# Kernel optimization log

Hardware: AMD Instinct MI355X
Metric: run time of the kernel (lower is better)

The kernel has to match this reference:

```python
import jax, jax.numpy as jnp
import numpy as np


def setup_inputs() -> dict:
    key = jax.random.key(0)
    ks = jax.random.split(key, 8)
    B, C, H, W = 8, 256, 64, 64
    Cqk = C // 8
    x = jax.random.normal(ks[0], (B, C, H, W), dtype=jnp.float32)
    # 1x1 conv weights, stored as [out_ch, in_ch] (kernel is 1x1)
    Wq = jax.random.normal(ks[1], (Cqk, C), dtype=jnp.float32) * 0.02
    bq = jnp.zeros((Cqk,), dtype=jnp.float32)
    Wk = jax.random.normal(ks[2], (Cqk, C), dtype=jnp.float32) * 0.02
    bk = jnp.zeros((Cqk,), dtype=jnp.float32)
    Wv = jax.random.normal(ks[3], (C, C), dtype=jnp.float32) * 0.02
    bv = jnp.zeros((C,), dtype=jnp.float32)
    # gamma initialized to zero in the module; use small nonzero so grads flow through attention path meaningfully
    gamma = jnp.asarray([0.5], dtype=jnp.float32)
    return {"x": x, "Wq": Wq, "bq": bq, "Wk": Wk, "bk": bk, "Wv": Wv, "bv": bv, "gamma": gamma}


def reference(x, Wq, bq, Wk, bk, Wv, bv, gamma):
    B, C, H, W = x.shape
    N = H * W
    xf = x.reshape(B, C, N)  # [B, C, N]
    # 1x1 convs == channel-wise matmuls
    q = jnp.einsum('oc,bcn->bno', Wq, xf) + bq  # [B, N, Cqk]
    k = jnp.einsum('oc,bcn->bon', Wk, xf) + bk[None, :, None]  # [B, Cqk, N]
    v = jnp.einsum('oc,bcn->bon', Wv, xf) + bv[None, :, None]  # [B, C, N]
    energy = jnp.einsum('bnd,bdm->bnm', q, k)  # [B, N, N], unscaled as in original
    attn = jax.nn.softmax(energy, axis=-1)
    out = jnp.einsum('bcm,bnm->bcn', v, attn)  # out[:, :, n] = sum_m v[:, :, m] * attn[n, m]
    out = out.reshape(B, C, H, W)
    return gamma[0] * out + x
```

## Files before the change

### kernel.cpp

```cpp
#include <hip/hip_runtime.h>
#include <hip/hip_bf16.h>

#define NB 8
#define CH 256
#define NN 4096
#define CQK 32
#define LOG2E 1.4426950408889634f

typedef __attribute__((ext_vector_type(4))) float f32x4;
typedef __attribute__((ext_vector_type(16))) float f32x16;
typedef __attribute__((ext_vector_type(8))) short bf16x8;
typedef unsigned short u16;

static __device__ __forceinline__ u16 f2bf(float f) {
  unsigned int u = __float_as_uint(f);
  unsigned int r = (u + 0x7fffu + ((u >> 16) & 1u)) >> 16;
  return (u16)r;
}

__global__ void prep_weights(const float* __restrict__ Wq, const float* __restrict__ bq,
                             const float* __restrict__ Wk, const float* __restrict__ bk,
                             const float* __restrict__ Wv,
                             u16* __restrict__ Wqkf, u16* __restrict__ Wvf,
                             float* __restrict__ bqk) {
  int i = blockIdx.x * 256 + threadIdx.x;
  int o = i >> 8, c = i & 255;
  int kk = c >> 5, g2 = (c >> 3) & 3, j = c & 7;
  if (o < 64) {
    float wv = (o < 32) ? Wq[o * 256 + c] * LOG2E : Wk[(o - 32) * 256 + c];
    Wqkf[((((o >> 4) * 8 + kk) * 4 + g2) * 16 + (o & 15)) * 8 + j] = f2bf(wv);
  }
  Wvf[((((o >> 4) * 8 + kk) * 4 + g2) * 16 + (o & 15)) * 8 + j] = f2bf(Wv[i]);
  if (i < 64) bqk[i] = (i < 32) ? bq[i] * LOG2E : bk[i - 32];
}

__global__ __launch_bounds__(256, 2) void fused_proj(
    const float* __restrict__ x, const u16* __restrict__ Wqkf,
    const u16* __restrict__ Wvf, const float* __restrict__ bqk,
    const float* __restrict__ bv,
    u16* __restrict__ qbuf, u16* __restrict__ kbuf, u16* __restrict__ vbuf) {
  __shared__ __align__(128) char xt[64 * 512];
  const int b = blockIdx.y, n0 = blockIdx.x * 64;
  const int tid = threadIdx.x, w = tid >> 6, l = tid & 63, g = l >> 4, lr = l & 15;
  const f32x4 fzero = {0.f, 0.f, 0.f, 0.f};

  {
    const int nl = l, cl = w;
    const float* xp = x + (size_t)b * CH * NN + n0 + nl;
    char* xrow = xt + nl * 512;
    const int swz = (nl & 15) << 4;
#pragma unroll
    for (int p = 0; p < 32; ++p) {
      const int c = p * 8 + cl * 2;
      float f0 = xp[(size_t)c * NN], f1 = xp[(size_t)(c + 1) * NN];
      unsigned int pk = (unsigned int)f2bf(f0) | ((unsigned int)f2bf(f1) << 16);
      *(unsigned int*)(xrow + ((c * 2) ^ swz)) = pk;
    }
  }
  __syncthreads();

  const int aswz = lr << 4;

  {
    f32x4 acc[4];
#pragma unroll
    for (int ct = 0; ct < 4; ++ct) acc[ct] = fzero;
#pragma unroll
    for (int kk = 0; kk < 8; ++kk) {
      bf16x8 af = *(const bf16x8*)(xt + (w * 16 + lr) * 512 + ((kk * 64 + g * 16) ^ aswz));
#pragma unroll
      for (int ct = 0; ct < 4; ++ct) {
        bf16x8 bf = *(const bf16x8*)(Wqkf + (size_t)(((ct * 8 + kk) * 4 + g) * 16 + lr) * 8);
        acc[ct] = __builtin_amdgcn_mfma_f32_16x16x32_bf16(af, bf, acc[ct], 0, 0, 0);
      }
    }
#pragma unroll
    for (int ct = 0; ct < 4; ++ct) {
      const int col = ct * 16 + lr;
      const float bc = bqk[col];
#pragma unroll
      for (int r = 0; r < 4; ++r) {
        const int row = n0 + w * 16 + g * 4 + r;
        u16 h = f2bf(acc[ct][r] + bc);
        if (col < 32) qbuf[((size_t)(b * NN + row)) * 32 + col] = h;
        else          kbuf[((size_t)(b * NN + row)) * 32 + (col - 32)] = h;
      }
    }
  }

  {
    f32x4 vacc[4][4];
#pragma unroll
    for (int ct = 0; ct < 4; ++ct)
#pragma unroll
      for (int mt = 0; mt < 4; ++mt) vacc[ct][mt] = fzero;
#pragma unroll
    for (int kk = 0; kk < 8; ++kk) {
      bf16x8 bfm[4];
#pragma unroll
      for (int mt = 0; mt < 4; ++mt)
        bfm[mt] = *(const bf16x8*)(xt + (mt * 16 + lr) * 512 + ((kk * 64 + g * 16) ^ aswz));
#pragma unroll
      for (int ct = 0; ct < 4; ++ct) {
        bf16x8 af = *(const bf16x8*)(Wvf + (size_t)((((w * 4 + ct) * 8 + kk) * 4 + g) * 16 + lr) * 8);
#pragma unroll
        for (int mt = 0; mt < 4; ++mt)
          vacc[ct][mt] = __builtin_amdgcn_mfma_f32_16x16x32_bf16(af, bfm[mt], vacc[ct][mt], 0, 0, 0);
      }
    }
#pragma unroll
    for (int ct = 0; ct < 4; ++ct) {
#pragma unroll
      for (int mt = 0; mt < 4; ++mt) {
        const int m = n0 + mt * 16 + lr;
#pragma unroll
        for (int r = 0; r < 4; ++r) {
          const int ch = w * 64 + ct * 16 + g * 4 + r;
          vbuf[((size_t)(b * 128 + (m >> 5)) * 256 + ch) * 32 + (m & 31)] = f2bf(vacc[ct][mt][r] + bv[ch]);
        }
      }
    }
  }
}

#define KLOAD(t, sub) (*(const bf16x8*)(kp + (size_t)((((t) & 63) * 64) + (sub) * 16) * 32))
#define VLOAD32(mg, k16) (*(const bf16x8*)(vp32 + (size_t)((mg) & 127) * 8192 + (k16)))

#define EXPP(S, PW, MASK) {                                                                   \
  float e0 = __builtin_amdgcn_exp2f(S[0]);                                                    \
  float e1 = __builtin_amdgcn_exp2f(S[1]);                                                    \
  float e2 = __builtin_amdgcn_exp2f(S[2]);                                                    \
  float e3 = __builtin_amdgcn_exp2f(S[3]);                                                    \
  lsum += (MASK) * ((e0 + e1) + (e2 + e3));                                                   \
  PW.x = __builtin_amdgcn_perm(__float_as_uint(e1) + 0x8000u, __float_as_uint(e0) + 0x8000u, 0x07060302u); \
  PW.y = __builtin_amdgcn_perm(__float_as_uint(e3) + 0x8000u, __float_as_uint(e2) + 0x8000u, 0x07060302u); \
}

#define PBAR() do {                                  \
  __builtin_amdgcn_sched_barrier(0);                 \
  asm volatile("s_waitcnt lgkmcnt(0)");              \
  __builtin_amdgcn_s_barrier();                      \
  __builtin_amdgcn_sched_barrier(0);                 \
} while (0)

#define PVPHASE32(BUF, V00, V01, V10, V11) {                                                  \
  const char* prb = (const char*)Pb + (BUF) * 16384;                                          \
  char* pdst = (char*)Pb + ((BUF) ^ 1) * 16384 + prow * 128;                                  \
  *(uint2*)(pdst + ((0 * 32 + g * 8) ^ wswz)) = pw0;                                          \
  *(uint2*)(pdst + ((1 * 32 + g * 8) ^ wswz)) = pw1;                                          \
  *(uint2*)(pdst + ((2 * 32 + g * 8) ^ wswz)) = pw2;                                          \
  *(uint2*)(pdst + ((3 * 32 + g * 8) ^ wswz)) = pw3;                                          \
  __builtin_amdgcn_s_setprio(1);                                                              \
  _Pragma("unroll")                                                                           \
  for (int qt = 0; qt < 4; ++qt) {                                                            \
    const int row = qt * 32 + (l & 31);                                                       \
    const int rs = (row & 7) << 4;                                                            \
    const char* base = prb + row * 128;                                                       \
    bf16x8 p00 = *(const bf16x8*)(base + ((0 + hi16) ^ rs));                                  \
    bf16x8 p01 = *(const bf16x8*)(base + ((32 + hi16) ^ rs));                                 \
    bf16x8 p10 = *(const bf16x8*)(base + ((64 + hi16) ^ rs));                                 \
    bf16x8 p11 = *(const bf16x8*)(base + ((96 + hi16) ^ rs));                                 \
    oacc32[qt] = __builtin_amdgcn_mfma_f32_32x32x16_bf16(V00, p00, oacc32[qt], 0, 0, 0);      \
    oacc32[qt] = __builtin_amdgcn_mfma_f32_32x32x16_bf16(V01, p01, oacc32[qt], 0, 0, 0);      \
    oacc32[qt] = __builtin_amdgcn_mfma_f32_32x32x16_bf16(V10, p10, oacc32[qt], 0, 0, 0);      \
    oacc32[qt] = __builtin_amdgcn_mfma_f32_32x32x16_bf16(V11, p11, oacc32[qt], 0, 0, 0);      \
  }                                                                                           \
  __builtin_amdgcn_s_setprio(0);                                                              \
}

__global__ __launch_bounds__(512, 2) void attn_fused(
    const u16* __restrict__ qb, const u16* __restrict__ kbuf,
    const u16* __restrict__ vbuf, const float* __restrict__ x,
    const float* __restrict__ gamma_p, float* __restrict__ out) {
  __shared__ __align__(128) char Pb[2][128 * 128];
  __shared__ float lsum_s[128];

  const int b = blockIdx.x;
  const int n0 = blockIdx.y * 128;
  const int tid = threadIdx.x, w = tid >> 6, l = tid & 63, g = l >> 4, lr = l & 15;
  const float gamma0 = gamma_p[0];
  const f32x4 fzero = {0.f, 0.f, 0.f, 0.f};
  const int hi16 = (l >> 5) << 4;

  bf16x8 qf = *(const bf16x8*)(qb + ((size_t)b * NN + n0 + w * 16 + lr) * 32 + g * 8);

  const u16* kp = kbuf + (size_t)b * (NN * 32) + (size_t)lr * 32 + g * 8;
  const u16* vp32 = vbuf + (size_t)b * 1048576 + (size_t)(w * 32 + (l & 31)) * 32 + (l >> 5) * 8;

  f32x16 oacc32[4];
#pragma unroll
  for (int qt = 0; qt < 4; ++qt) oacc32[qt] = (f32x16){};
  float lsum = 0.f;

  const int prow = w * 16 + lr;
  const int wswz = (prow & 7) << 4;

  bf16x8 kA0 = KLOAD(0, 0), kA1 = KLOAD(0, 1), kA2 = KLOAD(0, 2), kA3 = KLOAD(0, 3);
  bf16x8 vA0 = VLOAD32(0, 0), vA1 = VLOAD32(0, 16), vA2 = VLOAD32(1, 0), vA3 = VLOAD32(1, 16);
  bf16x8 kB0 = KLOAD(1, 0), kB1 = KLOAD(1, 1), kB2 = KLOAD(1, 2), kB3 = KLOAD(1, 3);
  bf16x8 vB0, vB1, vB2, vB3;
  uint2 pw0, pw1, pw2, pw3;
  {
    f32x4 s0 = __builtin_amdgcn_mfma_f32_16x16x32_bf16(kA0, qf, fzero, 0, 0, 0);
    f32x4 s1 = __builtin_amdgcn_mfma_f32_16x16x32_bf16(kA1, qf, fzero, 0, 0, 0);
    f32x4 s2 = __builtin_amdgcn_mfma_f32_16x16x32_bf16(kA2, qf, fzero, 0, 0, 0);
    f32x4 s3 = __builtin_amdgcn_mfma_f32_16x16x32_bf16(kA3, qf, fzero, 0, 0, 0);
    EXPP(s0, pw0, 1.0f); EXPP(s1, pw1, 1.0f); EXPP(s2, pw2, 1.0f); EXPP(s3, pw3, 1.0f);
    char* pdst = (char*)Pb + prow * 128;
    *(uint2*)(pdst + ((0 * 32 + g * 8) ^ wswz)) = pw0;
    *(uint2*)(pdst + ((1 * 32 + g * 8) ^ wswz)) = pw1;
    *(uint2*)(pdst + ((2 * 32 + g * 8) ^ wswz)) = pw2;
    *(uint2*)(pdst + ((3 * 32 + g * 8) ^ wswz)) = pw3;
  }

  for (int it2 = 0; it2 < 32; ++it2) {
    {
      const int tn = 2 * it2 + 1;
      f32x4 s0 = __builtin_amdgcn_mfma_f32_16x16x32_bf16(kB0, qf, fzero, 0, 0, 0);
      f32x4 s1 = __builtin_amdgcn_mfma_f32_16x16x32_bf16(kB1, qf, fzero, 0, 0, 0);
      f32x4 s2 = __builtin_amdgcn_mfma_f32_16x16x32_bf16(kB2, qf, fzero, 0, 0, 0);
      f32x4 s3 = __builtin_amdgcn_mfma_f32_16x16x32_bf16(kB3, qf, fzero, 0, 0, 0);
      kA0 = KLOAD(tn + 1, 0); kA1 = KLOAD(tn + 1, 1); kA2 = KLOAD(tn + 1, 2); kA3 = KLOAD(tn + 1, 3);
      vB0 = VLOAD32(2 * tn, 0); vB1 = VLOAD32(2 * tn, 16);
      vB2 = VLOAD32(2 * tn + 1, 0); vB3 = VLOAD32(2 * tn + 1, 16);
      EXPP(s0, pw0, 1.0f); EXPP(s1, pw1, 1.0f); EXPP(s2, pw2, 1.0f); EXPP(s3, pw3, 1.0f);
      PBAR();
      PVPHASE32(0, vA0, vA1, vA2, vA3);
    }
    {
      const int tn = 2 * it2 + 2;
      const float tmask = (it2 < 31) ? 1.0f : 0.0f;
      f32x4 s0 = __builtin_amdgcn_mfma_f32_16x16x32_bf16(kA0, qf, fzero, 0, 0, 0);
      f32x4 s1 = __builtin_amdgcn_mfma_f32_16x16x32_bf16(kA1, qf, fzero, 0, 0, 0);
      f32x4 s2 = __builtin_amdgcn_mfma_f32_16x16x32_bf16(kA2, qf, fzero, 0, 0, 0);
      f32x4 s3 = __builtin_amdgcn_mfma_f32_16x16x32_bf16(kA3, qf, fzero, 0, 0, 0);
      kB0 = KLOAD(tn + 1, 0); kB1 = KLOAD(tn + 1, 1); kB2 = KLOAD(tn + 1, 2); kB3 = KLOAD(tn + 1, 3);
      vA0 = VLOAD32(2 * tn, 0); vA1 = VLOAD32(2 * tn, 16);
      vA2 = VLOAD32(2 * tn + 1, 0); vA3 = VLOAD32(2 * tn + 1, 16);
      EXPP(s0, pw0, tmask); EXPP(s1, pw1, tmask); EXPP(s2, pw2, tmask); EXPP(s3, pw3, tmask);
      PBAR();
      PVPHASE32(1, vB0, vB1, vB2, vB3);
    }
  }

  lsum += __shfl_xor(lsum, 16);
  lsum += __shfl_xor(lsum, 32);
  if (l < 16) lsum_s[w * 16 + lr] = lsum;
  __syncthreads();

  const size_t bbase = (size_t)b * CH * NN;
#pragma unroll
  for (int qt = 0; qt < 4; ++qt) {
    const int q = qt * 32 + (l & 31);
    const float linv = 1.f / lsum_s[q];
    const int n = n0 + q;
#pragma unroll
    for (int a = 0; a < 4; ++a) {
#pragma unroll
      for (int rr = 0; rr < 4; ++rr) {
        const int ch = w * 32 + rr + a * 8 + 4 * (l >> 5);
        const size_t off = bbase + (size_t)ch * NN + n;
        out[off] = gamma0 * (oacc32[qt][a * 4 + rr] * linv) + x[off];
      }
    }
  }
}

extern "C" void kernel_launch(void* const* d_in, const int* in_sizes, int n_in,
                              void* d_out, int out_size, void* d_ws, size_t ws_size,
                              hipStream_t stream) {
  const float* x     = (const float*)d_in[0];
  const float* Wq    = (const float*)d_in[1];
  const float* bq    = (const float*)d_in[2];
  const float* Wk    = (const float*)d_in[3];
  const float* bk    = (const float*)d_in[4];
  const float* Wv    = (const float*)d_in[5];
  const float* bv    = (const float*)d_in[6];
  const float* gamma = (const float*)d_in[7];
  float* out = (float*)d_out;

  char* ws = (char*)d_ws;
  u16*   qbuf = (u16*)(ws);
  u16*   kbuf = (u16*)(ws + 2097152);
  u16*   vbuf = (u16*)(ws + 4194304);
  u16*   Wqkf = (u16*)(ws + 20971520);
  u16*   Wvf  = (u16*)(ws + 21004288);
  float* bqk  = (float*)(ws + 21135360);

  prep_weights<<<256, 256, 0, stream>>>(Wq, bq, Wk, bk, Wv, Wqkf, Wvf, bqk);
  fused_proj<<<dim3(64, 8), 256, 0, stream>>>(x, Wqkf, Wvf, bqk, bv, qbuf, kbuf, vbuf);
  attn_fused<<<dim3(8, 32), 512, 0, stream>>>(qbuf, kbuf, vbuf, x, gamma, out);
}
```

Before: 115.1 us.

## Retile PV stage to 16x16x32 MFMA with 2x4 wave grid over queries and channels

The PV product moves from 32x32x16 MFMAs, where each wave owned 32 channels across all 128 query rows, to 16x16x32 MFMAs over a 2x4 wave grid: 64 query rows by 64 channels per wave. Each P fragment read from LDS is now reused across four channel tiles, and V is loaded per channel tile, with the next V group's loads issued mid-phase. The goal is to cut LDS reads of P per MFMA and change how V loads overlap with compute. In exchange it uses more, smaller MFMAs, a different accumulator layout, and an altered V prefetch schedule.

```diff
diff --git a/kernel.cpp b/kernel.cpp
--- a/kernel.cpp
+++ b/kernel.cpp
@@ -8,7 +8,6 @@
 #define LOG2E 1.4426950408889634f
 
 typedef __attribute__((ext_vector_type(4))) float f32x4;
-typedef __attribute__((ext_vector_type(16))) float f32x16;
 typedef __attribute__((ext_vector_type(8))) short bf16x8;
 typedef unsigned short u16;
 
@@ -124,7 +123,7 @@
 }
 
 #define KLOAD(t, sub) (*(const bf16x8*)(kp + (size_t)((((t) & 63) * 64) + (sub) * 16) * 32))
-#define VLOAD32(mg, k16) (*(const bf16x8*)(vp32 + (size_t)((mg) & 127) * 8192 + (k16)))
+#define VLOAD(mg, ct) (*(const bf16x8*)(vp + (size_t)((mg) & 127) * 8192 + (ct) * 512))
 
 #define EXPP(S, PW, MASK) {                                                                   \
   float e0 = __builtin_amdgcn_exp2f(S[0]);                                                    \
@@ -143,7 +142,7 @@
   __builtin_amdgcn_sched_barrier(0);                 \
 } while (0)
 
-#define PVPHASE32(BUF, V00, V01, V10, V11) {                                                  \
+#define PVPH(BUF, NEXTMG) {                                                                   \
   const char* prb = (const char*)Pb + (BUF) * 16384;                                          \
   char* pdst = (char*)Pb + ((BUF) ^ 1) * 16384 + prow * 128;                                  \
   *(uint2*)(pdst + ((0 * 32 + g * 8) ^ wswz)) = pw0;                                          \
@@ -152,18 +151,26 @@
   *(uint2*)(pdst + ((3 * 32 + g * 8) ^ wswz)) = pw3;                                          \
   __builtin_amdgcn_s_setprio(1);                                                              \
   _Pragma("unroll")                                                                           \
-  for (int qt = 0; qt < 4; ++qt) {                                                            \
-    const int row = qt * 32 + (l & 31);                                                       \
+  for (int nt = 0; nt < 4; ++nt) {                                                            \
+    const int row = qg * 64 + nt * 16 + lr;                                                   \
     const int rs = (row & 7) << 4;                                                            \
-    const char* base = prb + row * 128;                                                       \
-    bf16x8 p00 = *(const bf16x8*)(base + ((0 + hi16) ^ rs));                                  \
-    bf16x8 p01 = *(const bf16x8*)(base + ((32 + hi16) ^ rs));                                 \
-    bf16x8 p10 = *(const bf16x8*)(base + ((64 + hi16) ^ rs));                                 \
-    bf16x8 p11 = *(const bf16x8*)(base + ((96 + hi16) ^ rs));                                 \
-    oacc32[qt] = __builtin_amdgcn_mfma_f32_32x32x16_bf16(V00, p00, oacc32[qt], 0, 0, 0);      \
-    oacc32[qt] = __builtin_amdgcn_mfma_f32_32x32x16_bf16(V01, p01, oacc32[qt], 0, 0, 0);      \
-    oacc32[qt] = __builtin_amdgcn_mfma_f32_32x32x16_bf16(V10, p10, oacc32[qt], 0, 0, 0);      \
-    oacc32[qt] = __builtin_amdgcn_mfma_f32_32x32x16_bf16(V11, p11, oacc32[qt], 0, 0, 0);      \
+    bf16x8 pa = *(const bf16x8*)(prb + row * 128 + ((g * 16) ^ rs));                          \
+    oacc[nt][0] = __builtin_amdgcn_mfma_f32_16x16x32_bf16(vA0, pa, oacc[nt][0], 0, 0, 0);     \
+    oacc[nt][1] = __builtin_amdgcn_mfma_f32_16x16x32_bf16(vA1, pa, oacc[nt][1], 0, 0, 0);     \
+    oacc[nt][2] = __builtin_amdgcn_mfma_f32_16x16x32_bf16(vA2, pa, oacc[nt][2], 0, 0, 0);     \
+    oacc[nt][3] = __builtin_amdgcn_mfma_f32_16x16x32_bf16(vA3, pa, oacc[nt][3], 0, 0, 0);     \
+  }                                                                                           \
+  vA0 = VLOAD(NEXTMG, 0); vA1 = VLOAD(NEXTMG, 1);                                             \
+  vA2 = VLOAD(NEXTMG, 2); vA3 = VLOAD(NEXTMG, 3);                                             \
+  _Pragma("unroll")                                                                           \
+  for (int nt = 0; nt < 4; ++nt) {                                                            \
+    const int row = qg * 64 + nt * 16 + lr;                                                   \
+    const int rs = (row & 7) << 4;                                                            \
+    bf16x8 pa = *(const bf16x8*)(prb + row * 128 + ((64 + g * 16) ^ rs));                     \
+    oacc[nt][0] = __builtin_amdgcn_mfma_f32_16x16x32_bf16(vB0, pa, oacc[nt][0], 0, 0, 0);     \
+    oacc[nt][1] = __builtin_amdgcn_mfma_f32_16x16x32_bf16(vB1, pa, oacc[nt][1], 0, 0, 0);     \
+    oacc[nt][2] = __builtin_amdgcn_mfma_f32_16x16x32_bf16(vB2, pa, oacc[nt][2], 0, 0, 0);     \
+    oacc[nt][3] = __builtin_amdgcn_mfma_f32_16x16x32_bf16(vB3, pa, oacc[nt][3], 0, 0, 0);     \
   }                                                                                           \
   __builtin_amdgcn_s_setprio(0);                                                              \
 }
@@ -178,25 +185,27 @@
   const int b = blockIdx.x;
   const int n0 = blockIdx.y * 128;
   const int tid = threadIdx.x, w = tid >> 6, l = tid & 63, g = l >> 4, lr = l & 15;
+  const int qg = w >> 2, cg = w & 3;
   const float gamma0 = gamma_p[0];
   const f32x4 fzero = {0.f, 0.f, 0.f, 0.f};
-  const int hi16 = (l >> 5) << 4;
 
   bf16x8 qf = *(const bf16x8*)(qb + ((size_t)b * NN + n0 + w * 16 + lr) * 32 + g * 8);
 
   const u16* kp = kbuf + (size_t)b * (NN * 32) + (size_t)lr * 32 + g * 8;
-  const u16* vp32 = vbuf + (size_t)b * 1048576 + (size_t)(w * 32 + (l & 31)) * 32 + (l >> 5) * 8;
-
-  f32x16 oacc32[4];
-#pragma unroll
-  for (int qt = 0; qt < 4; ++qt) oacc32[qt] = (f32x16){};
+  const u16* vp = vbuf + (size_t)b * 1048576 + (size_t)(cg * 64 + lr) * 32 + g * 8;
+
+  f32x4 oacc[4][4];
+#pragma unroll
+  for (int nt = 0; nt < 4; ++nt)
+#pragma unroll
+    for (int ct = 0; ct < 4; ++ct) oacc[nt][ct] = fzero;
   float lsum = 0.f;
 
   const int prow = w * 16 + lr;
   const int wswz = (prow & 7) << 4;
 
   bf16x8 kA0 = KLOAD(0, 0), kA1 = KLOAD(0, 1), kA2 = KLOAD(0, 2), kA3 = KLOAD(0, 3);
-  bf16x8 vA0 = VLOAD32(0, 0), vA1 = VLOAD32(0, 16), vA2 = VLOAD32(1, 0), vA3 = VLOAD32(1, 16);
+  bf16x8 vA0 = VLOAD(0, 0), vA1 = VLOAD(0, 1), vA2 = VLOAD(0, 2), vA3 = VLOAD(0, 3);
   bf16x8 kB0 = KLOAD(1, 0), kB1 = KLOAD(1, 1), kB2 = KLOAD(1, 2), kB3 = KLOAD(1, 3);
   bf16x8 vB0, vB1, vB2, vB3;
   uint2 pw0, pw1, pw2, pw3;
@@ -221,11 +230,11 @@
       f32x4 s2 = __builtin_amdgcn_mfma_f32_16x16x32_bf16(kB2, qf, fzero, 0, 0, 0);
       f32x4 s3 = __builtin_amdgcn_mfma_f32_16x16x32_bf16(kB3, qf, fzero, 0, 0, 0);
       kA0 = KLOAD(tn + 1, 0); kA1 = KLOAD(tn + 1, 1); kA2 = KLOAD(tn + 1, 2); kA3 = KLOAD(tn + 1, 3);
-      vB0 = VLOAD32(2 * tn, 0); vB1 = VLOAD32(2 * tn, 16);
-      vB2 = VLOAD32(2 * tn + 1, 0); vB3 = VLOAD32(2 * tn + 1, 16);
+      vB0 = VLOAD(4 * it2 + 1, 0); vB1 = VLOAD(4 * it2 + 1, 1);
+      vB2 = VLOAD(4 * it2 + 1, 2); vB3 = VLOAD(4 * it2 + 1, 3);
       EXPP(s0, pw0, 1.0f); EXPP(s1, pw1, 1.0f); EXPP(s2, pw2, 1.0f); EXPP(s3, pw3, 1.0f);
       PBAR();
-      PVPHASE32(0, vA0, vA1, vA2, vA3);
+      PVPH(0, 4 * it2 + 2);
     }
     {
       const int tn = 2 * it2 + 2;
@@ -235,11 +244,11 @@
       f32x4 s2 = __builtin_amdgcn_mfma_f32_16x16x32_bf16(kA2, qf, fzero, 0, 0, 0);
       f32x4 s3 = __builtin_amdgcn_mfma_f32_16x16x32_bf16(kA3, qf, fzero, 0, 0, 0);
       kB0 = KLOAD(tn + 1, 0); kB1 = KLOAD(tn + 1, 1); kB2 = KLOAD(tn + 1, 2); kB3 = KLOAD(tn + 1, 3);
-      vA0 = VLOAD32(2 * tn, 0); vA1 = VLOAD32(2 * tn, 16);
-      vA2 = VLOAD32(2 * tn + 1, 0); vA3 = VLOAD32(2 * tn + 1, 16);
+      vB0 = VLOAD(4 * it2 + 3, 0); vB1 = VLOAD(4 * it2 + 3, 1);
+      vB2 = VLOAD(4 * it2 + 3, 2); vB3 = VLOAD(4 * it2 + 3, 3);
       EXPP(s0, pw0, tmask); EXPP(s1, pw1, tmask); EXPP(s2, pw2, tmask); EXPP(s3, pw3, tmask);
       PBAR();
-      PVPHASE32(1, vB0, vB1, vB2, vB3);
+      PVPH(1, 4 * it2 + 4);
     }
   }
 
@@ -250,17 +259,17 @@
 
   const size_t bbase = (size_t)b * CH * NN;
 #pragma unroll
-  for (int qt = 0; qt < 4; ++qt) {
-    const int q = qt * 32 + (l & 31);
+  for (int nt = 0; nt < 4; ++nt) {
+    const int q = qg * 64 + nt * 16 + lr;
     const float linv = 1.f / lsum_s[q];
     const int n = n0 + q;
 #pragma unroll
-    for (int a = 0; a < 4; ++a) {
-#pragma unroll
-      for (int rr = 0; rr < 4; ++rr) {
-        const int ch = w * 32 + rr + a * 8 + 4 * (l >> 5);
-        const size_t off = bbase + (size_t)ch * NN + n;
-        out[off] = gamma0 * (oacc32[qt][a * 4 + rr] * linv) + x[off];
+    for (int ct = 0; ct < 4; ++ct) {
+      const int cbase = cg * 64 + ct * 16 + g * 4;
+#pragma unroll
+      for (int r = 0; r < 4; ++r) {
+        const size_t off = bbase + (size_t)(cbase + r) * NN + n;
+        out[off] = gamma0 * (oacc[nt][ct][r] * linv) + x[off];
       }
     }
   }
```

New measurement: 127.0 us. +10.4%, slower.
